# Kernel tuning notes

Measured on AMD Instinct MI355X. Metric: run time of the kernel, lower is better.

## Reference

```python
import jax, jax.numpy as jnp
import numpy as np

B, L, D = 4, 4096, 1024
NEG_BIG = -1e30  # finite stand-in for log(0) to keep vjp NaN-free; exp underflows to 0


def log_g(x):
    # log of g(x) = where(x>=0, x+0.5, sigmoid(x)); log-space, branch-safe
    return jnp.where(x >= 0.0, jnp.log(jax.nn.relu(x) + 0.5), -jax.nn.softplus(-x))


def setup_inputs() -> dict:
    key = jax.random.key(0)
    ks = jax.random.split(key, 4)
    std = np.sqrt(2.0 / D)  # kaiming_normal for fan_in = D
    x = jax.random.normal(ks[0], (B, L, D), dtype=jnp.float32)
    W_f = jax.random.normal(ks[1], (D, D), dtype=jnp.float32) * std
    W_i = jax.random.normal(ks[2], (D, D), dtype=jnp.float32) * std
    W_h = jax.random.normal(ks[3], (D, D), dtype=jnp.float32) * std
    b_f = jnp.zeros((D,), dtype=jnp.float32)
    b_i = jnp.zeros((D,), dtype=jnp.float32)
    b_h = jnp.zeros((D,), dtype=jnp.float32)
    return {"x": x, "W_f": W_f, "b_f": b_f, "W_i": W_i, "b_i": b_i, "W_h": W_h, "b_h": b_h}


def reference(x, W_f, b_f, W_i, b_i, W_h, b_h):
    # gate pre-activations: (B, L, D)
    f_pre = jnp.einsum('bld,ed->ble', x, W_f) + b_f
    i_pre = jnp.einsum('bld,ed->ble', x, W_i) + b_i
    h_pre = jnp.einsum('bld,ed->ble', x, W_h) + b_h

    # log-space normalized gates: log_f + log_i parametrize f/(f+i), i/(f+i)
    diff = jax.nn.softplus(-f_pre) - jax.nn.softplus(-i_pre)
    log_f = -jax.nn.softplus(diff)
    log_i = -jax.nn.softplus(-diff)
    log_tilde_h = log_g(h_pre)

    b, l, d = x.shape
    log_h0 = jnp.full((b, 1, d), NEG_BIG, dtype=x.dtype)  # log(0)
    log_values = jnp.concatenate([log_h0, log_i + log_tilde_h], axis=1)  # (B, L+1, D)

    # associative parallel scan in log space
    a_star = jnp.pad(jnp.cumsum(log_f, axis=1), ((0, 0), (1, 0), (0, 0)))  # (B, L+1, D)
    log_h = a_star + jax.lax.cumlogsumexp(log_values - a_star, axis=1)
    return jnp.exp(log_h)[:, 1:]  # (B, L, D)
```

## Files before the change

### kernel.cpp

```cpp
#include <hip/hip_runtime.h>

#define M_TOTAL 16384
#define N_DIM   1024
#define K_DIM   1024
#define L_SEQ   4096
#define B_SZ    4
#define D_DIM   1024
#define CH      64
#define NCHUNK  (L_SEQ / CH)
#define NCHAN   (B_SZ * D_DIM)

#define BM 128
#define BN 128
#define BK 64
#define NKT (K_DIM / BK)
#define TPB 512

typedef __attribute__((ext_vector_type(8))) short v8s;
typedef __attribute__((ext_vector_type(4))) float f32x4;

#define SB0()   __builtin_amdgcn_sched_barrier(0)
#define BAR()   __builtin_amdgcn_s_barrier()
#define WAITL0() do { asm volatile("s_waitcnt lgkmcnt(0)" ::: "memory"); SB0(); } while (0)
#define WAITL4() do { asm volatile("s_waitcnt lgkmcnt(4)" ::: "memory"); SB0(); } while (0)
#define WAITV0() do { asm volatile("s_waitcnt vmcnt(0)"   ::: "memory"); SB0(); } while (0)
#define AS1 __attribute__((address_space(1)))
#define AS3 __attribute__((address_space(3)))

__device__ __forceinline__ ushort f2b(float f) {
  uint u = __float_as_uint(f);
  u += 0x7FFFu + ((u >> 16) & 1u);
  return (ushort)(u >> 16);
}
__device__ __forceinline__ float b2f(ushort u) {
  return __uint_as_float(((uint)u) << 16);
}

__global__ void cast_f32_bf16(const float* __restrict__ src, ushort* __restrict__ dst, int n4) {
  int i = blockIdx.x * blockDim.x + threadIdx.x;
  if (i >= n4) return;
  float4 v = reinterpret_cast<const float4*>(src)[i];
  ushort4 o = make_ushort4(f2b(v.x), f2b(v.y), f2b(v.z), f2b(v.w));
  reinterpret_cast<ushort4*>(dst)[i] = o;
}

__global__ void cast_w3(const float* __restrict__ s0, const float* __restrict__ s1,
                        const float* __restrict__ s2,
                        ushort* __restrict__ o0, ushort* __restrict__ o1, ushort* __restrict__ o2) {
  int i = blockIdx.x * blockDim.x + threadIdx.x;
  const float* s = (blockIdx.y == 0) ? s0 : (blockIdx.y == 1) ? s1 : s2;
  ushort* o      = (blockIdx.y == 0) ? o0 : (blockIdx.y == 1) ? o1 : o2;
  float4 v = reinterpret_cast<const float4*>(s)[i];
  ushort4 t = make_ushort4(f2b(v.x), f2b(v.y), f2b(v.z), f2b(v.w));
  reinterpret_cast<ushort4*>(o)[i] = t;
}

__device__ __forceinline__ void gates(float fp, float ip, float hp, float& a, float& v) {
  float Ef = __expf(-fp);
  float Ei = __expf(-ip);
  float r  = __builtin_amdgcn_rcpf(2.f + Ef + Ei);
  float f  = (1.f + Ei) * r;
  float i  = (1.f + Ef) * r;
  float ht = (hp >= 0.f) ? (hp + 0.5f) : __builtin_amdgcn_rcpf(1.f + __expf(-hp));
  a = f;
  v = i * ht;
}

__launch_bounds__(TPB, 2)
__global__ void gemm_fused(const ushort* __restrict__ X,
                           const ushort* __restrict__ W0, const ushort* __restrict__ W1,
                           const ushort* __restrict__ W2,
                           const float* __restrict__ bfp, const float* __restrict__ bip,
                           const float* __restrict__ bhp,
                           uint* __restrict__ Pav,
                           float* __restrict__ AggA, float* __restrict__ AggV)
{
  __shared__ ushort lds[2][4][BM * BK];

  const int id  = blockIdx.x;
  const int sw  = (id & 7) * 128 + (id >> 3);
  const int n0  = (sw & 7) * BN;
  const int m0  = (sw >> 3) * BM;

  const int tid  = threadIdx.x;
  const int lane = tid & 63;
  const int w    = tid >> 6;
  const int wr   = w >> 2;
  const int wc   = w & 3;
  const int fr   = lane & 15, g = lane >> 4;

  int aoffh[4][2], boffh[2][2];
#pragma unroll
  for (int q = 0; q < 4; ++q)
#pragma unroll
    for (int ks = 0; ks < 2; ++ks) {
      int row = wr * 64 + q * 16 + fr;
      aoffh[q][ks] = row * BK + (((ks * 4 + g) ^ (row & 7)) << 3);
    }
#pragma unroll
  for (int n = 0; n < 2; ++n)
#pragma unroll
    for (int ks = 0; ks < 2; ++ks) {
      int row = wc * 32 + n * 16 + fr;
      boffh[n][ks] = row * BK + (((ks * 4 + g) ^ (row & 7)) << 3);
    }

  const int s0 = tid, s1 = 512 + tid;
  const int r0 = s0 >> 3, k0 = (s0 & 7) ^ (r0 & 7);
  const int r1 = s1 >> 3, k1 = (s1 & 7) ^ (r1 & 7);
  const int d0 = s0 * 8, d1 = s1 * 8;

  const ushort* gsrc[4][2];
  gsrc[0][0] = X  + (size_t)(m0 + r0) * K_DIM + k0 * 8;
  gsrc[0][1] = X  + (size_t)(m0 + r1) * K_DIM + k1 * 8;
  gsrc[1][0] = W0 + (size_t)(n0 + r0) * K_DIM + k0 * 8;
  gsrc[1][1] = W0 + (size_t)(n0 + r1) * K_DIM + k1 * 8;
  gsrc[2][0] = W1 + (size_t)(n0 + r0) * K_DIM + k0 * 8;
  gsrc[2][1] = W1 + (size_t)(n0 + r1) * K_DIM + k1 * 8;
  gsrc[3][0] = W2 + (size_t)(n0 + r0) * K_DIM + k0 * 8;
  gsrc[3][1] = W2 + (size_t)(n0 + r1) * K_DIM + k1 * 8;

  auto issue = [&](int buf, int mat, int kt, int j) {
    const ushort* s_ = gsrc[mat][j] + kt * BK;
    __builtin_amdgcn_global_load_lds((const AS1 void*)s_,
        (AS3 void*)(&lds[buf][mat][j ? d1 : d0]), 16, 0, 0);
  };

  f32x4 acc[3][4][2] = {};

#pragma unroll
  for (int mat = 0; mat < 4; ++mat) { issue(0, mat, 0, 0); issue(0, mat, 0, 1); }
  WAITV0();
  BAR(); SB0();

  int cur = 0;
  for (int t = 0; t < NKT; ++t) {
    const bool pf = (t + 1 < NKT);
    const ushort* rb = &lds[cur][0][0];
    v8s aF[4][2], bA[2][2], bB[2][2];

#pragma unroll
    for (int q = 0; q < 4; ++q)
#pragma unroll
      for (int ks = 0; ks < 2; ++ks)
        aF[q][ks] = *reinterpret_cast<const v8s*>(rb + aoffh[q][ks]);
#pragma unroll
    for (int n = 0; n < 2; ++n)
#pragma unroll
      for (int ks = 0; ks < 2; ++ks)
        bA[n][ks] = *reinterpret_cast<const v8s*>(rb + 1 * BM * BK + boffh[n][ks]);
    SB0();
    if (pf) {
#pragma unroll
      for (int mat = 0; mat < 4; ++mat) { issue(cur ^ 1, mat, t + 1, 0); issue(cur ^ 1, mat, t + 1, 1); }
    }
    SB0();
#pragma unroll
    for (int n = 0; n < 2; ++n)
#pragma unroll
      for (int ks = 0; ks < 2; ++ks)
        bB[n][ks] = *reinterpret_cast<const v8s*>(rb + 2 * BM * BK + boffh[n][ks]);
    SB0();
    WAITL4();
    __builtin_amdgcn_s_setprio(1);
#pragma unroll
    for (int ks = 0; ks < 2; ++ks)
#pragma unroll
      for (int mi = 0; mi < 4; ++mi) {
        acc[0][mi][0] = __builtin_amdgcn_mfma_f32_16x16x32_bf16(aF[mi][ks], bA[0][ks], acc[0][mi][0], 0, 0, 0);
        acc[0][mi][1] = __builtin_amdgcn_mfma_f32_16x16x32_bf16(aF[mi][ks], bA[1][ks], acc[0][mi][1], 0, 0, 0);
      }
    __builtin_amdgcn_s_setprio(0);
#pragma unroll
    for (int n = 0; n < 2; ++n)
#pragma unroll
      for (int ks = 0; ks < 2; ++ks)
        bA[n][ks] = *reinterpret_cast<const v8s*>(rb + 3 * BM * BK + boffh[n][ks]);
    SB0();
    WAITL4();
    __builtin_amdgcn_s_setprio(1);
#pragma unroll
    for (int ks = 0; ks < 2; ++ks)
#pragma unroll
      for (int mi = 0; mi < 4; ++mi) {
        acc[1][mi][0] = __builtin_amdgcn_mfma_f32_16x16x32_bf16(aF[mi][ks], bB[0][ks], acc[1][mi][0], 0, 0, 0);
        acc[1][mi][1] = __builtin_amdgcn_mfma_f32_16x16x32_bf16(aF[mi][ks], bB[1][ks], acc[1][mi][1], 0, 0, 0);
      }
    __builtin_amdgcn_s_setprio(0);
    WAITL0();
    __builtin_amdgcn_s_setprio(1);
#pragma unroll
    for (int ks = 0; ks < 2; ++ks)
#pragma unroll
      for (int mi = 0; mi < 4; ++mi) {
        acc[2][mi][0] = __builtin_amdgcn_mfma_f32_16x16x32_bf16(aF[mi][ks], bA[0][ks], acc[2][mi][0], 0, 0, 0);
        acc[2][mi][1] = __builtin_amdgcn_mfma_f32_16x16x32_bf16(aF[mi][ks], bA[1][ks], acc[2][mi][1], 0, 0, 0);
      }
    __builtin_amdgcn_s_setprio(0);

    if (pf) {
      WAITV0();
      BAR(); SB0();
      cur ^= 1;
    }
  }

  const int bidx = m0 >> 12;
  const int jch  = ((m0 & 4095) >> 6) + wr;
#pragma unroll
  for (int ni = 0; ni < 2; ++ni) {
    const int col = n0 + wc * 32 + ni * 16 + fr;
    const float vbf = bfp[col], vbi = bip[col], vbh = bhp[col];
    float BAgg[4], VAgg[4];
#pragma unroll
    for (int mi = 0; mi < 4; ++mi) {
      const int row0 = m0 + wr * 64 + mi * 16 + g * 4;
      float RA = 1.f, RV = 0.f;
#pragma unroll
      for (int r = 0; r < 4; ++r) {
        float a, v;
        gates(acc[0][mi][ni][r] + vbf, acc[1][mi][ni][r] + vbi, acc[2][mi][ni][r] + vbh, a, v);
        Pav[(size_t)(row0 + r) * N_DIM + col] = (uint)f2b(a) | ((uint)f2b(v) << 16);
        RA *= a; RV = fmaf(a, RV, v);
      }
      {
        float pA = __shfl_xor(RA, 16), pV = __shfl_xor(RV, 16);
        if (((lane >> 4) & 1) == 0) { RV = fmaf(pA, RV, pV); RA = RA * pA; }
        else                        { RV = fmaf(RA, pV, RV); RA = RA * pA; }
        pA = __shfl_xor(RA, 32); pV = __shfl_xor(RV, 32);
        if (((lane >> 5) & 1) == 0) { RV = fmaf(pA, RV, pV); RA = RA * pA; }
        else                        { RV = fmaf(RA, pV, RV); RA = RA * pA; }
      }
      BAgg[mi] = RA; VAgg[mi] = RV;
    }
    float CA = BAgg[0], CV = VAgg[0];
#pragma unroll
    for (int mi = 1; mi < 4; ++mi) { CV = fmaf(BAgg[mi], CV, VAgg[mi]); CA *= BAgg[mi]; }
    if (g == 0) {
      const int c = bidx * D_DIM + col;
      AggA[jch * NCHAN + c] = CA;
      AggV[jch * NCHAN + c] = CV;
    }
  }
}

__global__ void scan_mid(const float4* __restrict__ AggA, const float4* __restrict__ AggV,
                         float4* __restrict__ Start)
{
  int c4 = blockIdx.x * blockDim.x + threadIdx.x;
  float4 h = make_float4(0.f, 0.f, 0.f, 0.f);
#pragma unroll
  for (int j = 0; j < NCHUNK; ++j) {
    float4 A = AggA[(size_t)j * (NCHAN / 4) + c4];
    float4 V = AggV[(size_t)j * (NCHAN / 4) + c4];
    Start[(size_t)j * (NCHAN / 4) + c4] = h;
    h.x = fmaf(A.x, h.x, V.x);
    h.y = fmaf(A.y, h.y, V.y);
    h.z = fmaf(A.z, h.z, V.z);
    h.w = fmaf(A.w, h.w, V.w);
  }
}

__global__ void scan_pass2(const uint4* __restrict__ Pav4,
                           const float4* __restrict__ Start, float4* __restrict__ out4)
{
  int tid = blockIdx.x * blockDim.x + threadIdx.x;
  int c4 = tid & 1023;
  int chunk = tid >> 10;
  int b = c4 >> 8;
  int d4 = c4 & 255;
  size_t base4 = ((size_t)b * L_SEQ + (size_t)chunk * CH) * (D_DIM / 4) + d4;
  float4 h = Start[(size_t)chunk * (NCHAN / 4) + c4];
#pragma unroll 4
  for (int t = 0; t < CH; ++t) {
    size_t idx = base4 + (size_t)t * (D_DIM / 4);
    uint4 u = Pav4[idx];
    h.x = fmaf(b2f((ushort)(u.x & 0xFFFFu)), h.x, b2f((ushort)(u.x >> 16)));
    h.y = fmaf(b2f((ushort)(u.y & 0xFFFFu)), h.y, b2f((ushort)(u.y >> 16)));
    h.z = fmaf(b2f((ushort)(u.z & 0xFFFFu)), h.z, b2f((ushort)(u.z >> 16)));
    h.w = fmaf(b2f((ushort)(u.w & 0xFFFFu)), h.w, b2f((ushort)(u.w >> 16)));
    out4[idx] = h;
  }
}

extern "C" void kernel_launch(void* const* d_in, const int* in_sizes, int n_in,
                              void* d_out, int out_size, void* d_ws, size_t ws_size,
                              hipStream_t stream) {
  (void)in_sizes; (void)n_in; (void)out_size; (void)ws_size;
  const float* x  = (const float*)d_in[0];
  const float* Wf = (const float*)d_in[1];
  const float* bf = (const float*)d_in[2];
  const float* Wi = (const float*)d_in[3];
  const float* bi = (const float*)d_in[4];
  const float* Wh = (const float*)d_in[5];
  const float* bh = (const float*)d_in[6];

  ushort* xb  = (ushort*)d_ws;
  ushort* wfb = xb  + (size_t)M_TOTAL * K_DIM;
  ushort* wib = wfb + (size_t)N_DIM * K_DIM;
  ushort* whb = wib + (size_t)N_DIM * K_DIM;
  uint*  Pav  = (uint*)(whb + (size_t)N_DIM * K_DIM);
  float* AggA  = (float*)(Pav + (size_t)M_TOTAL * N_DIM);
  float* AggV  = AggA + NCHAN * NCHUNK;
  float* Start = AggV + NCHAN * NCHUNK;

  cast_f32_bf16<<<(M_TOTAL * K_DIM / 4) / 256, 256, 0, stream>>>(x, xb, M_TOTAL * K_DIM / 4);
  cast_w3<<<dim3((N_DIM * K_DIM / 4) / 256, 3), 256, 0, stream>>>(Wf, Wi, Wh, wfb, wib, whb);

  gemm_fused<<<dim3((M_TOTAL / BM) * (N_DIM / BN)), TPB, 0, stream>>>(
      xb, wfb, wib, whb, bf, bi, bh, Pav, AggA, AggV);

  scan_mid<<<(NCHAN / 4) / 256, 256, 0, stream>>>(
      (const float4*)AggA, (const float4*)AggV, (float4*)Start);
  scan_pass2<<<(NCHAN / 4 * NCHUNK) / 256, 256, 0, stream>>>(
      (const uint4*)Pav, (const float4*)Start, (float4*)d_out);
}
```

Baseline: 169.9 us.

## Fuse x fp32-to-bf16 cast into GEMM A-tile loading

Drops the separate cast kernel for x. The GEMM now loads fp32 x tiles into registers, converts them with packed bf16 conversion instructions and writes them to LDS itself, while the weight tiles keep using direct global-to-LDS loads. This removes one launch and a full write-and-reread of a 32 MB bf16 copy of x. In exchange, each GEMM block reads twice as many bytes for A, repeated across the 8 column blocks, and adds register pressure plus a synchronous LDS write before each barrier.

```diff
diff --git a/kernel.cpp b/kernel.cpp
--- a/kernel.cpp
+++ b/kernel.cpp
@@ -35,13 +35,10 @@
 __device__ __forceinline__ float b2f(ushort u) {
   return __uint_as_float(((uint)u) << 16);
 }
-
-__global__ void cast_f32_bf16(const float* __restrict__ src, ushort* __restrict__ dst, int n4) {
-  int i = blockIdx.x * blockDim.x + threadIdx.x;
-  if (i >= n4) return;
-  float4 v = reinterpret_cast<const float4*>(src)[i];
-  ushort4 o = make_ushort4(f2b(v.x), f2b(v.y), f2b(v.z), f2b(v.w));
-  reinterpret_cast<ushort4*>(dst)[i] = o;
+__device__ __forceinline__ uint cvtpk(float lo, float hi) {
+  uint r;
+  asm("v_cvt_pk_bf16_f32 %0, %1, %2" : "=v"(r) : "v"(lo), "v"(hi));
+  return r;
 }
 
 __global__ void cast_w3(const float* __restrict__ s0, const float* __restrict__ s1,
@@ -67,7 +64,7 @@
 }
 
 __launch_bounds__(TPB, 2)
-__global__ void gemm_fused(const ushort* __restrict__ X,
+__global__ void gemm_fused(const float* __restrict__ Xf,
                            const ushort* __restrict__ W0, const ushort* __restrict__ W1,
                            const ushort* __restrict__ W2,
                            const float* __restrict__ bfp, const float* __restrict__ bip,
@@ -110,27 +107,46 @@
   const int r1 = s1 >> 3, k1 = (s1 & 7) ^ (r1 & 7);
   const int d0 = s0 * 8, d1 = s1 * 8;
 
-  const ushort* gsrc[4][2];
-  gsrc[0][0] = X  + (size_t)(m0 + r0) * K_DIM + k0 * 8;
-  gsrc[0][1] = X  + (size_t)(m0 + r1) * K_DIM + k1 * 8;
-  gsrc[1][0] = W0 + (size_t)(n0 + r0) * K_DIM + k0 * 8;
-  gsrc[1][1] = W0 + (size_t)(n0 + r1) * K_DIM + k1 * 8;
-  gsrc[2][0] = W1 + (size_t)(n0 + r0) * K_DIM + k0 * 8;
-  gsrc[2][1] = W1 + (size_t)(n0 + r1) * K_DIM + k1 * 8;
-  gsrc[3][0] = W2 + (size_t)(n0 + r0) * K_DIM + k0 * 8;
-  gsrc[3][1] = W2 + (size_t)(n0 + r1) * K_DIM + k1 * 8;
-
-  auto issue = [&](int buf, int mat, int kt, int j) {
-    const ushort* s_ = gsrc[mat][j] + kt * BK;
+  const float* pxA0 = Xf + (size_t)(m0 + r0) * K_DIM + k0 * 8;
+  const float* pxA1 = Xf + (size_t)(m0 + r1) * K_DIM + k1 * 8;
+
+  const ushort* gsrcB[3][2];
+  gsrcB[0][0] = W0 + (size_t)(n0 + r0) * K_DIM + k0 * 8;
+  gsrcB[0][1] = W0 + (size_t)(n0 + r1) * K_DIM + k1 * 8;
+  gsrcB[1][0] = W1 + (size_t)(n0 + r0) * K_DIM + k0 * 8;
+  gsrcB[1][1] = W1 + (size_t)(n0 + r1) * K_DIM + k1 * 8;
+  gsrcB[2][0] = W2 + (size_t)(n0 + r0) * K_DIM + k0 * 8;
+  gsrcB[2][1] = W2 + (size_t)(n0 + r1) * K_DIM + k1 * 8;
+
+  auto issueB = [&](int buf, int zb, int kt, int j) {
+    const ushort* s_ = gsrcB[zb][j] + kt * BK;
     __builtin_amdgcn_global_load_lds((const AS1 void*)s_,
-        (AS3 void*)(&lds[buf][mat][j ? d1 : d0]), 16, 0, 0);
+        (AS3 void*)(&lds[buf][1 + zb][j ? d1 : d0]), 16, 0, 0);
   };
 
+  auto writeA = [&](int buf, const float4& a0, const float4& a1,
+                    const float4& a2, const float4& a3) {
+    uint4 u0, u1;
+    u0.x = cvtpk(a0.x, a0.y); u0.y = cvtpk(a0.z, a0.w);
+    u0.z = cvtpk(a1.x, a1.y); u0.w = cvtpk(a1.z, a1.w);
+    u1.x = cvtpk(a2.x, a2.y); u1.y = cvtpk(a2.z, a2.w);
+    u1.z = cvtpk(a3.x, a3.y); u1.w = cvtpk(a3.z, a3.w);
+    *reinterpret_cast<uint4*>(&lds[buf][0][d0]) = u0;
+    *reinterpret_cast<uint4*>(&lds[buf][0][d1]) = u1;
+  };
+
   f32x4 acc[3][4][2] = {};
-
-#pragma unroll
-  for (int mat = 0; mat < 4; ++mat) { issue(0, mat, 0, 0); issue(0, mat, 0, 1); }
+  float4 fA0, fA1, fA2, fA3;
+
+  fA0 = *reinterpret_cast<const float4*>(pxA0);
+  fA1 = *reinterpret_cast<const float4*>(pxA0 + 4);
+  fA2 = *reinterpret_cast<const float4*>(pxA1);
+  fA3 = *reinterpret_cast<const float4*>(pxA1 + 4);
+#pragma unroll
+  for (int zb = 0; zb < 3; ++zb) { issueB(0, zb, 0, 0); issueB(0, zb, 0, 1); }
   WAITV0();
+  writeA(0, fA0, fA1, fA2, fA3);
+  WAITL0();
   BAR(); SB0();
 
   int cur = 0;
@@ -151,8 +167,13 @@
         bA[n][ks] = *reinterpret_cast<const v8s*>(rb + 1 * BM * BK + boffh[n][ks]);
     SB0();
     if (pf) {
-#pragma unroll
-      for (int mat = 0; mat < 4; ++mat) { issue(cur ^ 1, mat, t + 1, 0); issue(cur ^ 1, mat, t + 1, 1); }
+      const int ko = (t + 1) * BK;
+      fA0 = *reinterpret_cast<const float4*>(pxA0 + ko);
+      fA1 = *reinterpret_cast<const float4*>(pxA0 + ko + 4);
+      fA2 = *reinterpret_cast<const float4*>(pxA1 + ko);
+      fA3 = *reinterpret_cast<const float4*>(pxA1 + ko + 4);
+#pragma unroll
+      for (int zb = 0; zb < 3; ++zb) { issueB(cur ^ 1, zb, t + 1, 0); issueB(cur ^ 1, zb, t + 1, 1); }
     }
     SB0();
 #pragma unroll
@@ -200,6 +221,8 @@
 
     if (pf) {
       WAITV0();
+      writeA(cur ^ 1, fA0, fA1, fA2, fA3);
+      WAITL0();
       BAR(); SB0();
       cur ^= 1;
     }
@@ -295,8 +318,7 @@
   const float* Wh = (const float*)d_in[5];
   const float* bh = (const float*)d_in[6];
 
-  ushort* xb  = (ushort*)d_ws;
-  ushort* wfb = xb  + (size_t)M_TOTAL * K_DIM;
+  ushort* wfb = (ushort*)d_ws;
   ushort* wib = wfb + (size_t)N_DIM * K_DIM;
   ushort* whb = wib + (size_t)N_DIM * K_DIM;
   uint*  Pav  = (uint*)(whb + (size_t)N_DIM * K_DIM);
@@ -304,11 +326,10 @@
   float* AggV  = AggA + NCHAN * NCHUNK;
   float* Start = AggV + NCHAN * NCHUNK;
 
-  cast_f32_bf16<<<(M_TOTAL * K_DIM / 4) / 256, 256, 0, stream>>>(x, xb, M_TOTAL * K_DIM / 4);
   cast_w3<<<dim3((N_DIM * K_DIM / 4) / 256, 3), 256, 0, stream>>>(Wf, Wi, Wh, wfb, wib, whb);
 
   gemm_fused<<<dim3((M_TOTAL / BM) * (N_DIM / BN)), TPB, 0, stream>>>(
-      xb, wfb, wib, whb, bf, bi, bh, Pav, AggA, AggV);
+      x, wfb, wib, whb, bf, bi, bh, Pav, AggA, AggV);
 
   scan_mid<<<(NCHAN / 4) / 256, 256, 0, stream>>>(
       (const float4*)AggA, (const float4*)AggV, (float4*)Start);
```

Result: faster. 164.2 us (-3.3%).
